# Performance work log

Hardware: AMD Instinct MI355X
Metric: run time of the kernel (lower is better)

The kernel has to match this reference:

```python
import jax, jax.numpy as jnp
import numpy as np

# Hyperparameters from init_kwargs
M = 32          # number of waveforms / antennas
N = 8192        # code length
T = 1e-3        # logsumexp temperature t
G = 0           # guard zone start
Ewin = N - 1    # guard zone end (E)
W = 0.1         # sidelobe weight


def _groupdiag():
    # Faithful to torch construction for the G == 0 branch:
    # start at (1-W), then overwrite columns [N-E, N-G) and column 0 with W.
    gd = (1.0 - W) * jnp.ones((M * M, N), dtype=jnp.float32)
    gd = gd.at[:, N - Ewin:N - G].set(W)
    gd = gd.at[:, 0:1].set(W)
    return gd


def setup_inputs() -> dict:
    key = jax.random.key(0)
    k1, _ = jax.random.split(key)
    # y_pred[0][:M*N] are normalized phases in [0,1); scaled by 2*pi inside.
    y_pred = jax.random.uniform(k1, (1, M * N), dtype=jnp.float32)
    y_true = jnp.zeros((1,), dtype=jnp.float32)  # unused by the loss
    return {"y_pred": y_pred, "y_true": y_true}


def _loss_and_stats(y_pred):
    x = y_pred[0][: M * N]
    # (N, M) phase matrix, unit-modulus complex waveform
    y = (2.0 * jnp.pi * x).reshape(M, N).T
    y_s = jnp.exp(1j * y)  # complex64, shape (N, M)
    # zero-padded FFT along time: (M, 2N)
    spec = jnp.fft.fft(y_s, n=2 * N, axis=0).T
    # torch: re1[r] = spec[r % M], re2[r] = spec[r // M];
    # sigma[r] = ifft(re1[r] * conj(re2[r]))
    # prod[a, b] = spec[b] * conj(spec[a]) so flattened row r = (a=r//M, b=r%M)
    prod = spec[None, :, :] * jnp.conj(spec)[:, None, :]          # (M, M, 2N)
    sigma = jnp.fft.ifft(prod.reshape(M * M, 2 * N), axis=1)      # (M*M, 2N)
    mag2 = jnp.abs(sigma) ** 2
    # cm[:,0] = |sigma[:,0]|^2 ; cm[:,1:] = |sigma[:,N+1:]|^2
    cm = jnp.concatenate([mag2[:, 0:1], mag2[:, N + 1:]], axis=1)  # (M*M, N)
    cm = cm * _groupdiag()
    idx_eye = np.arange(M) * M + np.arange(M)
    idx_oth = np.array([i * M + j for i in range(M) for j in range(M) if j != i])
    A = cm[idx_eye].T              # (N, M) autocorrelations
    APSL = A[1:].reshape(-1)       # drop zero-lag row
    CPSL = cm[idx_oth].T.reshape(-1)  # cross-correlations
    ac = jnp.concatenate([APSL, CPSL], axis=0) / N / N
    loss = T * jax.nn.logsumexp(ac / T)
    acd = jax.lax.stop_gradient(ac)
    Ad = jax.lax.stop_gradient(APSL)
    Cd = jax.lax.stop_gradient(CPSL)
    stats = (jnp.max(acd), jnp.max(Ad), jnp.max(Cd),
             jnp.sum(acd), jnp.sum(Ad), jnp.sum(Cd))
    return loss, stats


def reference(y_pred, y_true):
    loss, (PSL, APSL_o, CPSL_o, ISL, AISL, CISL) = _loss_and_stats(y_pred)
    return (loss, PSL, APSL_o, CPSL_o, ISL, AISL, CISL)
```

## Files before the change

### kernel.cpp

```cpp
#include <hip/hip_runtime.h>
#include <math.h>

#define M_WAVE 32
#define NLEN 8192
#define FFT_N 16384
#define NPAIR 528

#define TWOPI_F 6.28318530717958647692f

__device__ __forceinline__ float2 cadd(float2 a, float2 b){return make_float2(a.x+b.x, a.y+b.y);}
__device__ __forceinline__ float2 csub(float2 a, float2 b){return make_float2(a.x-b.x, a.y-b.y);}
__device__ __forceinline__ float2 cmul(float2 a, float2 b){return make_float2(a.x*b.x-a.y*b.y, a.x*b.y+a.y*b.x);}
__device__ __forceinline__ float2 mul_i (float2 a){return make_float2(-a.y,  a.x);}
__device__ __forceinline__ float2 mul_mi(float2 a){return make_float2( a.y, -a.x);}

__device__ __forceinline__ unsigned pkc(float2 v){
    unsigned r;
    asm("v_cvt_pk_bf16_f32 %0, %1, %2" : "=v"(r) : "v"(v.x), "v"(v.y));
    return r;
}
__device__ __forceinline__ float2 upkc(unsigned u){
    return make_float2(__uint_as_float(u << 16), __uint_as_float(u & 0xFFFF0000u));
}

__device__ __forceinline__ float2 dpp_xor1(float2 v){
    float2 r;
    r.x = __int_as_float(__builtin_amdgcn_mov_dpp(__float_as_int(v.x), 0xB1, 0xF, 0xF, true));
    r.y = __int_as_float(__builtin_amdgcn_mov_dpp(__float_as_int(v.y), 0xB1, 0xF, 0xF, true));
    return r;
}
__device__ __forceinline__ float2 dpp_xor2(float2 v){
    float2 r;
    r.x = __int_as_float(__builtin_amdgcn_mov_dpp(__float_as_int(v.x), 0x4E, 0xF, 0xF, true));
    r.y = __int_as_float(__builtin_amdgcn_mov_dpp(__float_as_int(v.y), 0x4E, 0xF, 0xF, true));
    return r;
}

__device__ __forceinline__ float waveReduceMax(float v) {
    #pragma unroll
    for (int off = 32; off > 0; off >>= 1) v = fmaxf(v, __shfl_down(v, off, 64));
    return v;
}
__device__ __forceinline__ float waveReduceSum(float v) {
    #pragma unroll
    for (int off = 32; off > 0; off >>= 1) v += __shfl_down(v, off, 64);
    return v;
}

template<int SGN>
__device__ __forceinline__ void dft16_tail(float2 w[16], float2 v[16]){
    const float C1 = 0.923879532511286756f;
    const float S1 = 0.382683432365089772f;
    const float R2 = 0.707106781186547524f;
    const float G = (SGN < 0) ? -1.0f : 1.0f;
    w[5]  = cmul(w[5],  make_float2( C1,  G*S1));
    w[6]  = cmul(w[6],  make_float2( R2,  G*R2));
    w[7]  = cmul(w[7],  make_float2( S1,  G*C1));
    w[9]  = cmul(w[9],  make_float2( R2,  G*R2));
    w[10] = (SGN<0) ? mul_mi(w[10]) : mul_i(w[10]);
    w[11] = cmul(w[11], make_float2(-R2,  G*R2));
    w[13] = cmul(w[13], make_float2( S1,  G*C1));
    w[14] = cmul(w[14], make_float2(-R2,  G*R2));
    w[15] = cmul(w[15], make_float2(-C1, -G*S1));
    #pragma unroll
    for (int k0 = 0; k0 < 4; ++k0){
        float2 a = w[k0*4+0], b = w[k0*4+1], c = w[k0*4+2], d = w[k0*4+3];
        float2 t0 = cadd(a,c), t1 = csub(a,c), t2 = cadd(b,d), t3 = csub(b,d);
        float2 j3 = (SGN < 0) ? mul_mi(t3) : mul_i(t3);
        v[k0]    = cadd(t0,t2);
        v[k0+4]  = cadd(t1,j3);
        v[k0+8]  = csub(t0,t2);
        v[k0+12] = csub(t1,j3);
    }
}

template<int SGN>
__device__ __forceinline__ void dft16(float2 v[16]){
    float2 w[16];
    #pragma unroll
    for (int n0 = 0; n0 < 4; ++n0){
        float2 a = v[n0], b = v[n0+4], c = v[n0+8], d = v[n0+12];
        float2 t0 = cadd(a,c), t1 = csub(a,c), t2 = cadd(b,d), t3 = csub(b,d);
        float2 j3 = (SGN < 0) ? mul_mi(t3) : mul_i(t3);
        w[n0]    = cadd(t0,t2);
        w[4+n0]  = cadd(t1,j3);
        w[8+n0]  = csub(t0,t2);
        w[12+n0] = csub(t1,j3);
    }
    dft16_tail<SGN>(w, v);
}

__device__ __forceinline__ void dft16_zero8(float2 v[16]){
    float2 w[16];
    #pragma unroll
    for (int n0 = 0; n0 < 4; ++n0){
        float2 a = v[n0], b = v[n0+4];
        w[n0]    = cadd(a,b);
        w[4+n0]  = make_float2(a.x + b.y, a.y - b.x);
        w[8+n0]  = csub(a,b);
        w[12+n0] = make_float2(a.x - b.y, a.y + b.x);
    }
    dft16_tail<-1>(w, v);
}

template<int SGN>
__device__ __forceinline__ void dft16_ip(float2 v[16]){
    const float C1 = 0.923879532511286756f;
    const float S1 = 0.382683432365089772f;
    const float R2 = 0.707106781186547524f;
    const float G = (SGN < 0) ? -1.0f : 1.0f;
    #pragma unroll
    for (int n1 = 0; n1 < 4; ++n1){
        float2 a = v[n1], b = v[n1+4], c = v[n1+8], d = v[n1+12];
        float2 t0 = cadd(a,c), t1 = csub(a,c), t2 = cadd(b,d), t3 = csub(b,d);
        float2 j3 = (SGN < 0) ? mul_mi(t3) : mul_i(t3);
        v[n1]    = cadd(t0,t2);
        v[n1+4]  = cadd(t1,j3);
        v[n1+8]  = csub(t0,t2);
        v[n1+12] = csub(t1,j3);
    }
    v[5]  = cmul(v[5],  make_float2( C1,  G*S1));
    v[6]  = cmul(v[6],  make_float2( R2,  G*R2));
    v[7]  = cmul(v[7],  make_float2( S1,  G*C1));
    v[9]  = cmul(v[9],  make_float2( R2,  G*R2));
    v[10] = (SGN<0) ? mul_mi(v[10]) : mul_i(v[10]);
    v[11] = cmul(v[11], make_float2(-R2,  G*R2));
    v[13] = cmul(v[13], make_float2( S1,  G*C1));
    v[14] = cmul(v[14], make_float2(-R2,  G*R2));
    v[15] = cmul(v[15], make_float2(-C1, -G*S1));
    #pragma unroll
    for (int kl = 0; kl < 4; ++kl){
        float2 a = v[4*kl], b = v[4*kl+1], c = v[4*kl+2], d = v[4*kl+3];
        float2 t0 = cadd(a,c), t1 = csub(a,c), t2 = cadd(b,d), t3 = csub(b,d);
        float2 j3 = (SGN < 0) ? mul_mi(t3) : mul_i(t3);
        v[4*kl]   = cadd(t0,t2);
        v[4*kl+1] = cadd(t1,j3);
        v[4*kl+2] = csub(t0,t2);
        v[4*kl+3] = csub(t1,j3);
    }
}

template<int SGN>
__device__ __forceinline__ void twchain16(float2 v[16], float theta){
    float th = (SGN < 0) ? -theta : theta;
    float s1,c1; __sincosf(th, &s1, &c1);
    float s4,c4; __sincosf(4.0f*th, &s4, &c4);
    float2 w1 = make_float2(c1,s1), w4 = make_float2(c4,s4);
    float2 lo2 = cmul(w1,w1), lo3 = cmul(lo2,w1);
    float2 hi2 = cmul(w4,w4), hi3 = cmul(hi2,w4);
    float2 lo[4] = {make_float2(1.f,0.f), w1, lo2, lo3};
    float2 hi[4] = {make_float2(1.f,0.f), w4, hi2, hi3};
    #pragma unroll
    for (int s = 1; s < 16; ++s){
        v[s] = cmul(v[s], cmul(hi[s>>2], lo[s&3]));
    }
}

__device__ __forceinline__ int L1swz(int e){
    return (e & ~63) | (((e & 63) + ((e >> 6) & 15)) & 63);
}

__global__ __launch_bounds__(512, 2) void fwd_fft_kernel(const float* __restrict__ x,
                                                         unsigned* __restrict__ spec) {
    __shared__ float2 X8[8192];
    const int bx = blockIdx.x, m = bx >> 1, hf = bx & 1;
    const int tid = threadIdx.x;

    #pragma unroll 1
    for (int cc = 0; cc < 2; ++cc){
        const int j = cc*512 + tid;
        float2 v[16];
        #pragma unroll
        for (int s = 0; s < 8; ++s){
            float ph = TWOPI_F * x[m*NLEN + s*1024 + j];
            float sn,cs; __sincosf(ph,&sn,&cs);
            v[s] = make_float2(cs,sn);
        }
        dft16_zero8(v);
        const float th = TWOPI_F * (float)j / 16384.0f;
        float sb,cb; __sincosf(-(float)(8*hf)*th, &sb, &cb);
        float ss,cs2; __sincosf(-th, &ss, &cs2);
        float2 wcur = make_float2(cb,sb), wstep = make_float2(cs2,ss);
        #pragma unroll
        for (int d = 0; d < 8; ++d){
            X8[d*1024 + L1swz(j)] = cmul(v[8*hf + d], wcur);
            wcur = cmul(wcur, wstep);
        }
    }
    __syncthreads();

    const int wv = tid >> 6, jB = tid & 63;
    float2 v[16];
    #pragma unroll
    for (int t = 0; t < 16; ++t) v[t] = X8[wv*1024 + t*64 + ((jB + t) & 63)];
    dft16<-1>(v);
    twchain16<-1>(v, TWOPI_F * (float)jB / 1024.0f);
    #pragma unroll
    for (int sp = 0; sp < 16; ++sp) X8[wv*1024 + sp*64 + ((jB + 4*sp) & 63)] = v[sp];

    {
        const int bl = (tid & 63) >> 2, jC = tid & 3;
        #pragma unroll
        for (int a = 0; a < 16; ++a)
            v[a] = X8[wv*1024 + bl*64 + ((4*a + jC + 4*bl) & 63)];
        dft16<-1>(v);
        twchain16<-1>(v, TWOPI_F * (float)jC / 64.0f);
        const bool odd1 = (jC & 1) != 0;
        const bool odd2 = (jC & 2) != 0;
        #pragma unroll
        for (int e = 0; e < 16; ++e){
            float2 p = dpp_xor2(v[e]);
            float2 t = odd2 ? csub(p, v[e]) : cadd(v[e], p);
            float2 q = dpp_xor1(t);
            float2 re = odd1 ? csub(q, t) : cadd(t, q);
            float2 ro = odd1 ? cadd(q, mul_i(t)) : cadd(t, mul_mi(q));
            v[e] = odd2 ? ro : re;
        }
        const int u = ((jC & 1) << 1) | (jC >> 1);
        uint4* dst = (uint4*)(spec + (size_t)m*FFT_N + (8*hf + wv)*1024 + bl*64 + u*16);
        #pragma unroll
        for (int e = 0; e < 4; ++e)
            dst[e] = make_uint4(pkc(v[4*e]), pkc(v[4*e+1]), pkc(v[4*e+2]), pkc(v[4*e+3]));
    }
}

__global__ __launch_bounds__(512, 4) void pair_kernel(const unsigned* __restrict__ spec,
                                                      float4* __restrict__ rec) {
    __shared__ unsigned X[FFT_N];
    __shared__ float scr2[64];
    const int r = blockIdx.x, tid = threadIdx.x;
    const bool is_packed = (r >= 496);
    int a, b;
    if (is_packed){
        const int k = r - 496; a = 2*k; b = 2*k + 1;
    } else {
        int t = r; a = 0; int rem = M_WAVE - 1;
        while (t >= rem){ t -= rem; ++a; rem = M_WAVE - 1 - a; }
        b = a + 1 + t;
    }
    const int jC = tid & 3;
    const int u = ((jC & 1) << 1) | (jC >> 1);
    const bool odd1 = (jC & 1) != 0;
    const bool odd2 = (jC & 2) != 0;

    #pragma unroll
    for (int p = 0; p < 2; ++p){
        const int blk = (tid >> 2) + 128*p;
        float2 v[16];
        const uint4* pa = (const uint4*)(spec + (size_t)a*FFT_N + blk*64 + u*16);
        const uint4* pb = (const uint4*)(spec + (size_t)b*FFT_N + blk*64 + u*16);
        #pragma unroll
        for (int e = 0; e < 4; ++e){
            uint4 A = pa[e], B = pb[e];
            float2 a0 = upkc(A.x), a1 = upkc(A.y), a2 = upkc(A.z), a3 = upkc(A.w);
            float2 b0 = upkc(B.x), b1 = upkc(B.y), b2 = upkc(B.z), b3 = upkc(B.w);
            if (is_packed){
                v[4*e+0] = make_float2(a0.x*a0.x + a0.y*a0.y, b0.x*b0.x + b0.y*b0.y);
                v[4*e+1] = make_float2(a1.x*a1.x + a1.y*a1.y, b1.x*b1.x + b1.y*b1.y);
                v[4*e+2] = make_float2(a2.x*a2.x + a2.y*a2.y, b2.x*b2.x + b2.y*b2.y);
                v[4*e+3] = make_float2(a3.x*a3.x + a3.y*a3.y, b3.x*b3.x + b3.y*b3.y);
            } else {
                v[4*e+0] = make_float2(b0.x*a0.x + b0.y*a0.y, b0.y*a0.x - b0.x*a0.y);
                v[4*e+1] = make_float2(b1.x*a1.x + b1.y*a1.y, b1.y*a1.x - b1.x*a1.y);
                v[4*e+2] = make_float2(b2.x*a2.x + b2.y*a2.y, b2.y*a2.x - b2.x*a2.y);
                v[4*e+3] = make_float2(b3.x*a3.x + b3.y*a3.y, b3.y*a3.x - b3.x*a3.y);
            }
        }
        #pragma unroll
        for (int e = 0; e < 16; ++e){
            float2 q = dpp_xor1(v[e]);
            float2 t = odd1 ? csub(q, v[e]) : cadd(v[e], q);
            float2 pp = dpp_xor2(t);
            float2 re = odd2 ? csub(pp, t) : cadd(t, pp);
            float2 ro = odd2 ? csub(pp, mul_i(t)) : cadd(t, mul_i(pp));
            v[e] = odd1 ? ro : re;
        }
        twchain16<+1>(v, TWOPI_F * (float)jC / 64.0f);
        dft16_ip<+1>(v);
        const int rot = 4*(blk & 15);
        #pragma unroll
        for (int s = 0; s < 16; ++s){
            const int t = 4*(s&3) + (s>>2);
            X[blk*64 + ((4*t + jC + rot) & 63)] = pkc(v[s]);
        }
    }
    const int wv = tid >> 6, jB = tid & 63;
    #pragma unroll
    for (int p = 0; p < 2; ++p){
        const int sB = wv + 8*p;
        float2 v[16];
        #pragma unroll
        for (int sp = 0; sp < 16; ++sp) v[sp] = upkc(X[sB*1024 + sp*64 + ((jB + 4*sp) & 63)]);
        twchain16<+1>(v, TWOPI_F * (float)jB / 1024.0f);
        dft16_ip<+1>(v);
        #pragma unroll
        for (int s = 0; s < 16; ++s){
            const int t = 4*(s&3) + (s>>2);
            X[sB*1024 + t*64 + ((jB + t) & 63)] = pkc(v[s]);
        }
    }
    __syncthreads();

    const float CSCALE = 0.1f / (16384.0f * 16384.0f);
    const float invTN2 = 1.0f / 67108.864f;
    const int lane = tid & 63, wvv = tid >> 6;

    if (!is_packed){
        float uval[2][16];
        float lm = 0.f, lsum = 0.f;
        #pragma unroll
        for (int p = 0; p < 2; ++p){
            const int tp = tid + 512*p;
            const int baseA = L1swz(tp);
            float2 v[16];
            #pragma unroll
            for (int s = 0; s < 16; ++s) v[s] = upkc(X[s*1024 + baseA]);
            twchain16<+1>(v, TWOPI_F * (float)tp / 16384.0f);
            dft16_ip<+1>(v);
            const bool j0 = (tp == 0);
            #pragma unroll
            for (int s = 0; s < 16; ++s){
                const int t = 4*(s&3) + (s>>2);
                float uu = CSCALE * (v[s].x*v[s].x + v[s].y*v[s].y);
                uval[p][s] = uu;
                bool inv = (t == 8) && j0;
                if (!inv){ lm = fmaxf(lm, uu); lsum += uu; }
                if (t == 0 && j0) lsum += uu;
            }
        }
        __syncthreads();

        float* scratch = (float*)X;
        float wm = waveReduceMax(lm);
        float wsm = waveReduceSum(lsum);
        if (lane == 0){ scratch[wvv] = wm; scratch[8+wvv] = wsm; }
        __syncthreads();
        float m_b = scratch[0], sumu = scratch[8];
        #pragma unroll
        for (int i = 1; i < 8; ++i){ m_b = fmaxf(m_b, scratch[i]); sumu += scratch[8+i]; }

        float le = 0.f;
        #pragma unroll
        for (int p = 0; p < 2; ++p){
            const bool j0 = (p == 0) && (tid == 0);
            #pragma unroll
            for (int s = 0; s < 16; ++s){
                const int t = 4*(s&3) + (s>>2);
                float ex = __expf((uval[p][s] - m_b) * invTN2);
                bool inv = (t == 8) && j0;
                if (!inv) le += ((t == 0 && j0) ? 2.f : 1.f) * ex;
            }
        }
        float wle = waveReduceSum(le);
        if (lane == 0) scratch[16+wvv] = wle;
        __syncthreads();
        if (tid == 0){
            float sb2 = 0.f;
            #pragma unroll
            for (int i = 0; i < 8; ++i) sb2 += scratch[16+i];
            rec[M_WAVE + r] = make_float4(m_b, sumu, sb2, 0.f);
        }
    } else {
        unsigned zpk[2][16];
        #pragma unroll
        for (int p = 0; p < 2; ++p){
            const int tp = tid + 512*p;
            const int baseA = L1swz(tp);
            float2 v[16];
            #pragma unroll
            for (int s = 0; s < 16; ++s) v[s] = upkc(X[s*1024 + baseA]);
            twchain16<+1>(v, TWOPI_F * (float)tp / 16384.0f);
            dft16_ip<+1>(v);
            #pragma unroll
            for (int s = 0; s < 16; ++s) zpk[p][s] = pkc(v[s]);
        }
        __syncthreads();
        #pragma unroll
        for (int p = 0; p < 2; ++p){
            const int tp = tid + 512*p;
            #pragma unroll
            for (int s = 0; s < 16; ++s){
                const int t = 4*(s&3) + (s>>2);
                X[t*1024 + tp] = zpk[p][s];
            }
        }
        __syncthreads();

        float lma = 0.f, lmb = 0.f, lsa = 0.f, lsb = 0.f;
        #pragma unroll
        for (int p = 0; p < 2; ++p){
            const int tp = tid + 512*p;
            #pragma unroll
            for (int s = 0; s < 16; ++s){
                const int t = 4*(s&3) + (s>>2);
                if (t < 8) continue;
                if (t == 8 && tp == 0) continue;
                const int n = t*1024 + tp;
                float2 z  = upkc(X[n]);
                float2 zc = upkc(X[FFT_N - n]);
                float ar = 0.5f*(z.x + zc.x), ai = 0.5f*(z.y - zc.y);
                float br = 0.5f*(z.x - zc.x), bi = 0.5f*(z.y + zc.y);
                float ua = CSCALE*(ar*ar + ai*ai);
                float ub = CSCALE*(br*br + bi*bi);
                lma = fmaxf(lma, ua); lsa += ua;
                lmb = fmaxf(lmb, ub); lsb += ub;
            }
        }
        float wma = waveReduceMax(lma), wmb = waveReduceMax(lmb);
        float wsa = waveReduceSum(lsa), wsb = waveReduceSum(lsb);
        if (lane == 0){ scr2[wvv]=wma; scr2[8+wvv]=wmb; scr2[16+wvv]=wsa; scr2[24+wvv]=wsb; }
        __syncthreads();
        float m_a = scr2[0], m_b = scr2[8], s_a = scr2[16], s_b = scr2[24];
        #pragma unroll
        for (int i = 1; i < 8; ++i){
            m_a = fmaxf(m_a, scr2[i]);    m_b = fmaxf(m_b, scr2[8+i]);
            s_a += scr2[16+i];            s_b += scr2[24+i];
        }
        float lea = 0.f, leb = 0.f;
        #pragma unroll
        for (int p = 0; p < 2; ++p){
            const int tp = tid + 512*p;
            #pragma unroll
            for (int s = 0; s < 16; ++s){
                const int t = 4*(s&3) + (s>>2);
                if (t < 8) continue;
                if (t == 8 && tp == 0) continue;
                const int n = t*1024 + tp;
                float2 z  = upkc(X[n]);
                float2 zc = upkc(X[FFT_N - n]);
                float ar = 0.5f*(z.x + zc.x), ai = 0.5f*(z.y - zc.y);
                float br = 0.5f*(z.x - zc.x), bi = 0.5f*(z.y + zc.y);
                float ua = CSCALE*(ar*ar + ai*ai);
                float ub = CSCALE*(br*br + bi*bi);
                lea += __expf((ua - m_a)*invTN2);
                leb += __expf((ub - m_b)*invTN2);
            }
        }
        float wlea = waveReduceSum(lea), wleb = waveReduceSum(leb);
        if (lane == 0){ scr2[32+wvv] = wlea; scr2[40+wvv] = wleb; }
        __syncthreads();
        if (tid == 0){
            float ta = 0.f, tb = 0.f;
            #pragma unroll
            for (int i = 0; i < 8; ++i){ ta += scr2[32+i]; tb += scr2[40+i]; }
            const int k = r - 496;
            rec[2*k]   = make_float4(m_a, s_a, ta, 0.f);
            rec[2*k+1] = make_float4(m_b, s_b, tb, 0.f);
        }
    }
}

__global__ __launch_bounds__(64) void final_kernel(const float4* __restrict__ rec,
                                                   float* __restrict__ out) {
    const int lane = threadIdx.x;
    float mA = 0.f, mC = 0.f;
    for (int r = lane; r < NPAIR; r += 64){
        float mx = rec[r].x;
        if (r < M_WAVE) mA = fmaxf(mA, mx); else mC = fmaxf(mC, mx);
    }
    #pragma unroll
    for (int off = 32; off > 0; off >>= 1){
        mA = fmaxf(mA, __shfl_xor(mA, off, 64));
        mC = fmaxf(mC, __shfl_xor(mC, off, 64));
    }
    const float Mall = fmaxf(mA, mC);
    const float invTN2f = 1.0f / 67108.864f;
    double S = 0.0, sA = 0.0, sC = 0.0;
    for (int r = lane; r < NPAIR; r += 64){
        float4 rv = rec[r];
        S += (double)rv.z * (double)__expf((rv.x - Mall)*invTN2f);
        if (r < M_WAVE) sA += (double)rv.y; else sC += (double)rv.y;
    }
    #pragma unroll
    for (int off = 32; off > 0; off >>= 1){
        S  += __shfl_xor(S,  off, 64);
        sA += __shfl_xor(sA, off, 64);
        sC += __shfl_xor(sC, off, 64);
    }
    if (lane == 0){
        const double invN2 = 1.0/67108864.0;
        out[0] = (float)((double)Mall*invN2 + 1e-3*log(S));
        out[1] = (float)((double)Mall*invN2);
        out[2] = mA;
        out[3] = mC;
        out[4] = (float)((sA + sC)*invN2);
        out[5] = (float)sA;
        out[6] = (float)sC;
    }
}

extern "C" void kernel_launch(void* const* d_in, const int* in_sizes, int n_in,
                              void* d_out, int out_size, void* d_ws, size_t ws_size,
                              hipStream_t stream) {
    (void)in_sizes; (void)n_in; (void)out_size; (void)ws_size;
    const float* x = (const float*)d_in[0];
    float* out = (float*)d_out;

    unsigned* spec = (unsigned*)d_ws;
    float4* rec = (float4*)((char*)d_ws + (size_t)M_WAVE * FFT_N * sizeof(unsigned));

    fwd_fft_kernel<<<64, 512, 0, stream>>>(x, spec);
    pair_kernel<<<512, 512, 0, stream>>>(spec, rec);
    final_kernel<<<1, 64, 0, stream>>>(rec, out);
}
```

Measured before the change: 52.18 us.

## Split forward FFT into two kernels via bf16 global intermediate for more parallelism

The forward FFT kernel is split into a first-stage kernel that computes the zero-padded radix-16 stage and writes bf16-packed results to a global scratch buffer, and a second kernel that does the remaining two stages per 1024-chunk. The original kernel ran only 64 blocks, each duplicating the first stage across halves, and was limited by its large shared-memory footprint. The new layout launches 128 blocks per kernel with no redundant first-stage work. In exchange it adds a kernel launch, a global round trip, and extra bf16 rounding of the intermediate values.

```diff
diff --git a/kernel.cpp b/kernel.cpp
--- a/kernel.cpp
+++ b/kernel.cpp
@@ -160,49 +160,46 @@
     return (e & ~63) | (((e & 63) + ((e >> 6) & 15)) & 63);
 }
 
-__global__ __launch_bounds__(512, 2) void fwd_fft_kernel(const float* __restrict__ x,
-                                                         unsigned* __restrict__ spec) {
-    __shared__ float2 X8[8192];
-    const int bx = blockIdx.x, m = bx >> 1, hf = bx & 1;
+__global__ __launch_bounds__(256, 1) void stageA_kernel(const float* __restrict__ x,
+                                                        unsigned* __restrict__ mid) {
+    const int bx = blockIdx.x, m = bx >> 2, grp = bx & 3;
+    const int j = grp*256 + threadIdx.x;
+    float2 v[16];
+    #pragma unroll
+    for (int s = 0; s < 8; ++s){
+        float ph = TWOPI_F * x[m*NLEN + s*1024 + j];
+        float sn,cs; __sincosf(ph,&sn,&cs);
+        v[s] = make_float2(cs,sn);
+    }
+    dft16_zero8(v);
+    twchain16<-1>(v, TWOPI_F * (float)j / 16384.0f);
+    unsigned* dst = mid + (size_t)m*FFT_N + L1swz(j);
+    #pragma unroll
+    for (int s = 0; s < 16; ++s) dst[s*1024] = pkc(v[s]);
+}
+
+__global__ __launch_bounds__(256, 1) void bc_kernel(const unsigned* __restrict__ mid,
+                                                    unsigned* __restrict__ spec) {
+    __shared__ float2 X[4096];
+    const int bx = blockIdx.x, m = bx >> 2, g = bx & 3;
     const int tid = threadIdx.x;
-
-    #pragma unroll 1
-    for (int cc = 0; cc < 2; ++cc){
-        const int j = cc*512 + tid;
-        float2 v[16];
-        #pragma unroll
-        for (int s = 0; s < 8; ++s){
-            float ph = TWOPI_F * x[m*NLEN + s*1024 + j];
-            float sn,cs; __sincosf(ph,&sn,&cs);
-            v[s] = make_float2(cs,sn);
-        }
-        dft16_zero8(v);
-        const float th = TWOPI_F * (float)j / 16384.0f;
-        float sb,cb; __sincosf(-(float)(8*hf)*th, &sb, &cb);
-        float ss,cs2; __sincosf(-th, &ss, &cs2);
-        float2 wcur = make_float2(cb,sb), wstep = make_float2(cs2,ss);
-        #pragma unroll
-        for (int d = 0; d < 8; ++d){
-            X8[d*1024 + L1swz(j)] = cmul(v[8*hf + d], wcur);
-            wcur = cmul(wcur, wstep);
-        }
-    }
-    __syncthreads();
-
     const int wv = tid >> 6, jB = tid & 63;
+    const int ch = g*4 + wv;
+    const unsigned* base = mid + (size_t)m*FFT_N + ch*1024;
     float2 v[16];
-    #pragma unroll
-    for (int t = 0; t < 16; ++t) v[t] = X8[wv*1024 + t*64 + ((jB + t) & 63)];
+
+    #pragma unroll
+    for (int t = 0; t < 16; ++t) v[t] = upkc(base[t*64 + ((jB + t) & 63)]);
     dft16<-1>(v);
     twchain16<-1>(v, TWOPI_F * (float)jB / 1024.0f);
     #pragma unroll
-    for (int sp = 0; sp < 16; ++sp) X8[wv*1024 + sp*64 + ((jB + 4*sp) & 63)] = v[sp];
+    for (int sp = 0; sp < 16; ++sp) X[wv*1024 + sp*64 + ((jB + 4*sp) & 63)] = v[sp];
 
     {
         const int bl = (tid & 63) >> 2, jC = tid & 3;
         #pragma unroll
         for (int a = 0; a < 16; ++a)
-            v[a] = X8[wv*1024 + bl*64 + ((4*a + jC + 4*bl) & 63)];
+            v[a] = X[wv*1024 + bl*64 + ((4*a + jC + 4*bl) & 63)];
         dft16<-1>(v);
         twchain16<-1>(v, TWOPI_F * (float)jC / 64.0f);
         const bool odd1 = (jC & 1) != 0;
@@ -217,7 +214,7 @@
             v[e] = odd2 ? ro : re;
         }
         const int u = ((jC & 1) << 1) | (jC >> 1);
-        uint4* dst = (uint4*)(spec + (size_t)m*FFT_N + (8*hf + wv)*1024 + bl*64 + u*16);
+        uint4* dst = (uint4*)(spec + (size_t)m*FFT_N + ch*1024 + bl*64 + u*16);
         #pragma unroll
         for (int e = 0; e < 4; ++e)
             dst[e] = make_uint4(pkc(v[4*e]), pkc(v[4*e+1]), pkc(v[4*e+2]), pkc(v[4*e+3]));
@@ -497,9 +494,12 @@
     float* out = (float*)d_out;
 
     unsigned* spec = (unsigned*)d_ws;
-    float4* rec = (float4*)((char*)d_ws + (size_t)M_WAVE * FFT_N * sizeof(unsigned));
-
-    fwd_fft_kernel<<<64, 512, 0, stream>>>(x, spec);
+    float4* rec = (float4*)((char*)d_ws + (size_t)M_WAVE * FFT_N * 4);
+    unsigned* mid = (unsigned*)((char*)d_ws + (size_t)M_WAVE * FFT_N * 4
+                                + (size_t)NPAIR * sizeof(float4));
+
+    stageA_kernel<<<128, 256, 0, stream>>>(x, mid);
+    bc_kernel<<<128, 256, 0, stream>>>(mid, spec);
     pair_kernel<<<512, 512, 0, stream>>>(spec, rec);
     final_kernel<<<1, 64, 0, stream>>>(rec, out);
 }
```

Result: faster. 47.84 us (-8.3%).
